# Performance work log

Hardware: AMD Instinct MI355X
Metric: run time of the kernel (lower is better)

Reference implementation:

```python
import jax, jax.numpy as jnp
import numpy as np

BETA = 0.25


def setup_inputs() -> dict:
    key = jax.random.key(0)
    k1, k2, k3 = jax.random.split(key, 3)
    B, T, D, K = 4, 2048, 512, 16384
    z_e = jax.random.normal(k1, (B, T, D), dtype=jnp.float32)
    codebook = jax.random.normal(k2, (K, D), dtype=jnp.float32)  # frozen embedding
    # nn.Linear(D, D, bias=False) weight, scaled like kaiming-uniform magnitude
    W = jax.random.normal(k3, (D, D), dtype=jnp.float32) * (1.0 / np.sqrt(D))
    return {"z_e": z_e, "codebook": codebook, "W": W}


def reference(z_e, codebook, W):
    B, T, D = z_e.shape
    # effective codebook: Linear(codebook) = codebook @ W.T   -> (K, D)
    eff = jnp.matmul(codebook, W.T)
    z_flat = z_e.reshape(-1, D)  # (N, D)
    # squared euclidean distances (argmin-equivalent to cdist p=2)
    d2 = (
        jnp.sum(z_flat * z_flat, axis=1, keepdims=True)  # (N,1)
        - 2.0 * jnp.matmul(z_flat, eff.T)                  # (N,K)
        + jnp.sum(eff * eff, axis=1)[None, :]              # (1,K)
    )
    code_indices = jnp.argmin(d2, axis=1)  # (N,)
    z_q = eff[code_indices].reshape(B, T, D)
    loss_w = jnp.mean((jax.lax.stop_gradient(z_e) - z_q) ** 2)
    loss_commit = BETA * jnp.mean((z_e - jax.lax.stop_gradient(z_q)) ** 2)
    total_loss = loss_w + loss_commit
    # straight-through estimator
    z_q_out = z_e + jax.lax.stop_gradient(z_q - z_e)
    return z_q_out, total_loss, code_indices.reshape(B, T)
```

## Files before the change

kernel.cpp:

```cpp
#include <hip/hip_runtime.h>
#include <stdint.h>


#define N_ROWS 8192
#define DIM    512
#define K_CB   16384
#define TILE_F16 16384
#define HALF_F16 8192
#define KT_EFF 24
#define KT_D   8
#define PAN_D   ((size_t)KT_D * TILE_F16)
#define RMARGIN 4.0f

typedef _Float16 f16x8 __attribute__((ext_vector_type(8)));
typedef float f32x4 __attribute__((ext_vector_type(4)));

#define FENCE() asm volatile("" ::: "memory")
#define BARRIER() do { FENCE(); __builtin_amdgcn_s_barrier(); FENCE(); } while (0)
#define VMCNT(n) asm volatile("s_waitcnt vmcnt(" #n ")" ::: "memory")

__device__ __forceinline__ void gload_lds16(const void* g, void* l) {
  __builtin_amdgcn_global_load_lds(
      (const __attribute__((address_space(1))) uint32_t*)g,
      (__attribute__((address_space(3))) uint32_t*)l, 16, 0, 0);
}


__device__ __forceinline__ void stage_half(const _Float16* src, _Float16* ldsb,
                                           int w, int lane) {
  const _Float16* s = src + w * 512 + lane * 8;
  _Float16* l = ldsb + w * 512;
  gload_lds16(s, l);
  gload_lds16(s + 4096, l + 4096);
}

template <int MQ>
__device__ __forceinline__ void read_a(const _Float16* At, int wr, int lh, int lq,
                                       f16x8 af[4][2]) {
#pragma unroll
  for (int m2 = 0; m2 < 4; ++m2) {
    const int row = wr * 128 + (MQ * 4 + m2) * 16 + lh;
    const int half = row >> 7, r = row & 127;
#pragma unroll
    for (int kk = 0; kk < 2; ++kk) {
      const int kblk = kk * 4 + lq;
      af[m2][kk] = *reinterpret_cast<const f16x8*>(
          &At[(((size_t)(half * 8 + kblk)) * 128 + r) * 8]);
    }
  }
}

template <int NQ>
__device__ __forceinline__ void read_b(const _Float16* Bt, int wc, int lh, int lq,
                                       f16x8 bf[4][2]) {
#pragma unroll
  for (int n2 = 0; n2 < 2; ++n2) {
    const int row = wc * 64 + (NQ * 2 + n2) * 16 + lh;
    const int half = row >> 7, r = row & 127;
#pragma unroll
    for (int kk = 0; kk < 2; ++kk) {
      const int kblk = kk * 4 + lq;
      bf[NQ * 2 + n2][kk] = *reinterpret_cast<const f16x8*>(
          &Bt[(((size_t)(half * 8 + kblk)) * 128 + r) * 8]);
    }
  }
}

template <int MQ, int NQ>
__device__ __forceinline__ void mfma_phase(const f16x8 af[4][2],
                                           const f16x8 bf[4][2],
                                           f32x4 acc[8][4]) {
  __builtin_amdgcn_s_setprio(1);
#pragma unroll
  for (int m2 = 0; m2 < 4; ++m2)
#pragma unroll
    for (int n2 = 0; n2 < 2; ++n2)
#pragma unroll
      for (int kk = 0; kk < 2; ++kk)
        acc[MQ * 4 + m2][NQ * 2 + n2] = __builtin_amdgcn_mfma_f32_16x16x32_f16(
            af[m2][kk], bf[NQ * 2 + n2][kk], acc[MQ * 4 + m2][NQ * 2 + n2], 0, 0, 0);
  __builtin_amdgcn_s_setprio(0);
}

__device__ __forceinline__ void pipeline8(
    const _Float16* Abase, const _Float16* Bbase,
    _Float16 (&lds)[4][TILE_F16], f32x4 (&acc)[8][4],
    int w, int lane, int wr, int wc, int lh, int lq, int NT) {
  f16x8 af[4][2], bf[4][2];
  stage_half(Abase, &lds[0][0], w, lane);
  stage_half(Abase + HALF_F16, &lds[0][HALF_F16], w, lane);
  stage_half(Bbase, &lds[1][0], w, lane);
  stage_half(Bbase + HALF_F16, &lds[1][HALF_F16], w, lane);
  stage_half(Bbase + TILE_F16, &lds[3][0], w, lane);
  stage_half(Bbase + TILE_F16 + HALF_F16, &lds[3][HALF_F16], w, lane);
  stage_half(Abase + TILE_F16, &lds[2][0], w, lane);
  VMCNT(6);
  BARRIER();
  for (int t = 0; t < NT; ++t) {
    const int s = t & 1;
    const _Float16* At = &lds[s * 2 + 0][0];
    const _Float16* Bt = &lds[s * 2 + 1][0];
    read_a<0>(At, wr, lh, lq, af);
    read_b<0>(Bt, wc, lh, lq, bf);
    if (t + 1 < NT)
      stage_half(Abase + (size_t)(t + 1) * TILE_F16 + HALF_F16,
                 &lds[(s ^ 1) * 2][HALF_F16], w, lane);
    BARRIER();
    mfma_phase<0, 0>(af, bf, acc);
    BARRIER();
    read_b<1>(Bt, wc, lh, lq, bf);
    BARRIER();
    mfma_phase<0, 1>(af, bf, acc);
    BARRIER();
    read_a<1>(At, wr, lh, lq, af);
    if (t + 2 < NT)
      stage_half(Bbase + (size_t)(t + 2) * TILE_F16, &lds[s * 2 + 1][0], w, lane);
    BARRIER();
    mfma_phase<1, 1>(af, bf, acc);
    BARRIER();
    if (t + 2 < NT) {
      stage_half(Bbase + (size_t)(t + 2) * TILE_F16 + HALF_F16,
                 &lds[s * 2 + 1][HALF_F16], w, lane);
      stage_half(Abase + (size_t)(t + 2) * TILE_F16, &lds[s * 2][0], w, lane);
    }
    BARRIER();
    mfma_phase<1, 0>(af, bf, acc);
    if (t == NT - 2) { VMCNT(0); } else { VMCNT(6); }
    BARRIER();
  }
}

__global__ __launch_bounds__(256) void split_tiled_kernel(
    const float* __restrict__ S, _Float16* __restrict__ T, int resid_limb) {
  const int b = blockIdx.x;
  const int mp = b / 48;
  const int r1 = b % 48;
  const int kt = r1 >> 1, half = r1 & 1;
  const int limb = kt >> 3;
  const int ksrc = (kt & 7) * 64;
  const bool resid = (limb == resid_limb);
  const int t = threadIdx.x;
  _Float16* dst = T + ((size_t)(mp * KT_EFF + kt) * 2 + half) * HALF_F16;
#pragma unroll
  for (int cc = 0; cc < 4; ++cc) {
    const int ci = cc * 256 + t;
    const int kblk = ci >> 7, row = ci & 127;
    const int m = mp * 256 + half * 128 + row;
    const float* src = &S[(size_t)m * DIM + ksrc + kblk * 8];
    float4 x0 = *reinterpret_cast<const float4*>(src);
    float4 x1 = *reinterpret_cast<const float4*>(src + 4);
    const float xs[8] = {x0.x, x0.y, x0.z, x0.w, x1.x, x1.y, x1.z, x1.w};
    f16x8 o;
    if (!resid) {
#pragma unroll
      for (int j = 0; j < 8; ++j) o[j] = (_Float16)xs[j];
    } else {
#pragma unroll
      for (int j = 0; j < 8; ++j) {
        _Float16 h = (_Float16)xs[j];
        o[j] = (_Float16)(xs[j] - (float)h);
      }
    }
    *reinterpret_cast<f16x8*>(&dst[(size_t)ci * 8]) = o;
  }
}

__global__ __launch_bounds__(256) void split1_kernel(
    const float* __restrict__ S, _Float16* __restrict__ T) {
  const int b = blockIdx.x;
  const int p = b >> 4;
  const int r1 = b & 15;
  const int kt = r1 >> 1, half = r1 & 1;
  const int ksrc = kt * 64;
  const int t = threadIdx.x;
  _Float16* dst = T + ((size_t)(p * KT_D + kt) * 2 + half) * HALF_F16;
#pragma unroll
  for (int cc = 0; cc < 4; ++cc) {
    const int ci = cc * 256 + t;
    const int kblk = ci >> 7, row = ci & 127;
    const int m = p * 256 + half * 128 + row;
    const float* src = &S[(size_t)m * DIM + ksrc + kblk * 8];
    float4 x0 = *reinterpret_cast<const float4*>(src);
    float4 x1 = *reinterpret_cast<const float4*>(src + 4);
    const float xs[8] = {x0.x, x0.y, x0.z, x0.w, x1.x, x1.y, x1.z, x1.w};
    f16x8 o;
#pragma unroll
    for (int j = 0; j < 8; ++j) o[j] = (_Float16)xs[j];
    *reinterpret_cast<f16x8*>(&dst[(size_t)ci * 8]) = o;
  }
}

__global__ __launch_bounds__(256) void effgemm128_kernel(
    const _Float16* __restrict__ CpT, const _Float16* __restrict__ WpT,
    float* __restrict__ eff, _Float16* __restrict__ BpT) {
  __shared__ __align__(16) _Float16 lbuf[2][2][HALF_F16];
  const int tid = threadIdx.x;
  const int w = tid >> 6, lane = tid & 63;
  const int lh = lane & 15, lq = lane >> 4;
  const int wr = w >> 1, wc = w & 1;
  const int bid = blockIdx.x;
  const int nb = bid & 3, mh = bid >> 2;
  const int pA = mh >> 1, hA = mh & 1;
  const int pB = nb >> 1, hB = nb & 1;
  f32x4 acc[4][4] = {};

  auto stage = [&](int kt, int buf) {
    const _Float16* a = CpT + (((size_t)pA * KT_EFF + kt) * 2 + hA) * HALF_F16;
    const _Float16* b = WpT + (((size_t)pB * KT_EFF + kt) * 2 + hB) * HALF_F16;
#pragma unroll
    for (int i = 0; i < 4; ++i) {
      const int off = i * 2048 + w * 512;
      gload_lds16(a + off + lane * 8, &lbuf[buf][0][off]);
      gload_lds16(b + off + lane * 8, &lbuf[buf][1][off]);
    }
  };

  stage(0, 0);
  for (int kt = 0; kt < KT_EFF; ++kt) {
    __syncthreads();
    if (kt + 1 < KT_EFF) stage(kt + 1, (kt + 1) & 1);
    const _Float16* At = &lbuf[kt & 1][0][0];
    const _Float16* Bt = &lbuf[kt & 1][1][0];
    f16x8 af[4][2], bf[4][2];
#pragma unroll
    for (int mf = 0; mf < 4; ++mf) {
      const int r = wr * 64 + mf * 16 + lh;
#pragma unroll
      for (int kk = 0; kk < 2; ++kk)
        af[mf][kk] = *reinterpret_cast<const f16x8*>(
            &At[((kk * 4 + lq) * 128 + r) * 8]);
    }
#pragma unroll
    for (int nf = 0; nf < 4; ++nf) {
      const int r = wc * 64 + nf * 16 + lh;
#pragma unroll
      for (int kk = 0; kk < 2; ++kk)
        bf[nf][kk] = *reinterpret_cast<const f16x8*>(
            &Bt[((kk * 4 + lq) * 128 + r) * 8]);
    }
    __builtin_amdgcn_s_setprio(1);
#pragma unroll
    for (int mf = 0; mf < 4; ++mf)
#pragma unroll
      for (int nf = 0; nf < 4; ++nf)
#pragma unroll
        for (int kk = 0; kk < 2; ++kk)
          acc[mf][nf] = __builtin_amdgcn_mfma_f32_16x16x32_f16(
              af[mf][kk], bf[nf][kk], acc[mf][nf], 0, 0, 0);
    __builtin_amdgcn_s_setprio(0);
  }

#pragma unroll
  for (int mf = 0; mf < 4; ++mf)
#pragma unroll
    for (int nf = 0; nf < 4; ++nf)
#pragma unroll
      for (int j = 0; j < 4; ++j) {
        const int rl = wr * 64 + mf * 16 + lq * 4 + j;
        const int cl = wc * 64 + nf * 16 + lh;
        const int row = mh * 128 + rl;
        const int col = nb * 128 + cl;
        const float v = acc[mf][nf][j];
        eff[(size_t)row * DIM + col] = v;
        const int ktd = col >> 6, kblk = (col >> 3) & 7, ce = col & 7;
        BpT[((((size_t)(row >> 8) * KT_D + ktd) * 2 + ((row >> 7) & 1)) * 8 + kblk)
                * 1024 + (row & 127) * 8 + ce] = (_Float16)v;
      }
}

__global__ __launch_bounds__(256) void effnorm_kernel(
    const float* __restrict__ E, float* __restrict__ En) {
  const int w = threadIdx.x >> 6;
  const int lane = threadIdx.x & 63;
  const int row = blockIdx.x * 4 + w;
  const float* er = &E[(size_t)row * DIM];
  float s = 0.f;
#pragma unroll
  for (int k = 0; k < DIM / 64; ++k) {
    float v = er[lane + k * 64];
    s = fmaf(v, v, s);
  }
#pragma unroll
  for (int o = 32; o; o >>= 1) s += __shfl_down(s, o, 64);
  if (lane == 0) En[row] = s;
}

__global__ __launch_bounds__(512) void dist1_kernel(
    const _Float16* __restrict__ ApT, const _Float16* __restrict__ BpT,
    const float* __restrict__ En, float* __restrict__ gv,
    unsigned* __restrict__ gmask) {
  __shared__ __align__(16) _Float16 lds[4][TILE_F16];
  const int tid = threadIdx.x;
  const int w = tid >> 6, lane = tid & 63;
  const int lh = lane & 15, lq = lane >> 4;
  const int wr = w >> 2, wc = w & 3;
  const int bid = blockIdx.x;
  const int xcd = bid & 7, c = bid >> 3;
  const int np = xcd * 8 + (c & 7);
  const int mp = c >> 3;
  f32x4 acc[8][4] = {};
  pipeline8(ApT + (size_t)mp * PAN_D, BpT + (size_t)np * PAN_D, lds, acc,
            w, lane, wr, wc, lh, lq, KT_D);
  float en[4];
#pragma unroll
  for (int nf = 0; nf < 4; ++nf)
    en[nf] = En[np * 256 + wc * 64 + nf * 16 + lh];
#pragma unroll
  for (int mf = 0; mf < 8; ++mf) {
#pragma unroll
    for (int j = 0; j < 4; ++j) {
      const float s0 = fmaf(-2.f, acc[mf][0][j], en[0]);
      const float s1 = fmaf(-2.f, acc[mf][1][j], en[1]);
      const float s2 = fmaf(-2.f, acc[mf][2][j], en[2]);
      const float s3 = fmaf(-2.f, acc[mf][3][j], en[3]);
      float v0 = fminf(s0, s1);
      float v1 = fminf(s2, s3);
#pragma unroll
      for (int m = 1; m < 16; m <<= 1) {
        v0 = fminf(v0, __shfl_xor(v0, m, 64));
        v1 = fminf(v1, __shfl_xor(v1, m, 64));
      }
      const unsigned long long b0 = __ballot(s0 <= v0 + RMARGIN);
      const unsigned long long b1 = __ballot(s1 <= v0 + RMARGIN);
      const unsigned long long b2 = __ballot(s2 <= v1 + RMARGIN);
      const unsigned long long b3 = __ballot(s3 <= v1 + RMARGIN);
      if (lh == 0) {
        const int row = mp * 256 + wr * 128 + mf * 16 + lq * 4 + j;
        float* gp = &gv[(size_t)row * 512 + np * 8 + wc * 2];
        gp[0] = v0; gp[1] = v1;
        const unsigned w0 = (unsigned)((b0 >> (lq * 16)) & 0xFFFFull) |
                            ((unsigned)((b1 >> (lq * 16)) & 0xFFFFull) << 16);
        const unsigned w1 = (unsigned)((b2 >> (lq * 16)) & 0xFFFFull) |
                            ((unsigned)((b3 >> (lq * 16)) & 0xFFFFull) << 16);
        unsigned* mq = &gmask[(size_t)row * 512 + np * 8 + wc * 2];
        mq[0] = w0; mq[1] = w1;
      }
    }
  }
}

__global__ __launch_bounds__(256) void flag_kernel(
    const float* __restrict__ gv, int* __restrict__ fcnt,
    unsigned short* __restrict__ flist) {
  const int t = threadIdx.x;
  const int w = t >> 6, lane = t & 63;
  const int row = blockIdx.x * 4 + w;
  float v[8];
#pragma unroll
  for (int i = 0; i < 8; ++i) v[i] = gv[(size_t)row * 512 + i * 64 + lane];
  float A = v[0];
#pragma unroll
  for (int i = 1; i < 8; ++i) A = fminf(A, v[i]);
#pragma unroll
  for (int m = 1; m < 64; m <<= 1) A = fminf(A, __shfl_xor(A, m, 64));
  __shared__ int cnt[4];
  __shared__ unsigned short lst[4][64];
  if (lane == 0) cnt[w] = 0;
  __syncthreads();
  const float thr = A + RMARGIN;
#pragma unroll
  for (int i = 0; i < 8; ++i) {
    if (v[i] <= thr) {
      int p = atomicAdd(&cnt[w], 1);
      if (p < 64) lst[w][p] = (unsigned short)(i * 64 + lane);
    }
  }
  __syncthreads();
  const int cn = cnt[w];
  if (lane == 0) fcnt[row] = (cn > 64) ? -1 : cn;
  if (lane < cn && lane < 64) flist[(size_t)row * 64 + lane] = lst[w][lane];
}

__global__ __launch_bounds__(256) void refine_kernel(
    const float* __restrict__ Z, const float* __restrict__ E,
    const float* __restrict__ En, const int* __restrict__ fcnt,
    const unsigned short* __restrict__ flist, const unsigned* __restrict__ gmask,
    float* __restrict__ zq, float* __restrict__ out_idx,
    float* __restrict__ ploss) {
  const int row = blockIdx.x;
  const int t = threadIdx.x;
  const int w = t >> 6, lane = t & 63;
  const int hl = lane & 31;
  const int hi = lane >> 5;
  __shared__ float zrow[512];
  __shared__ unsigned short glist[512];
  __shared__ float bvs[4];
  __shared__ int bis[4];
  __shared__ int sidx;
  __shared__ float wsum[4];
  if (t < 128)
    ((float4*)zrow)[t] = ((const float4*)(Z + (size_t)row * 512))[t];
  const int cr = fcnt[row];
  int ng;
  if (cr < 0) {
    glist[t] = (unsigned short)t;
    glist[t + 256] = (unsigned short)(t + 256);
    ng = 512;
  } else {
    ng = cr;
    if (t < cr) glist[t] = flist[(size_t)row * 64 + t];
  }
  float4 zr0, zr1, zr2, zr3;
  {
    const float4* zp = (const float4*)(Z + (size_t)row * 512 + hl * 16);
    zr0 = zp[0]; zr1 = zp[1]; zr2 = zp[2]; zr3 = zp[3];
  }
  __syncthreads();

  float bv = 3.0e38f;
  int bi = 2147483647;
  for (int q = w; q < ng; q += 4) {
    const int g = glist[q];
    unsigned m = gmask[(size_t)row * 512 + g];
    while (m) {
      const int c0 = __builtin_ctz(m);
      m &= m - 1;
      int c1 = -1;
      if (m) { c1 = __builtin_ctz(m); m &= m - 1; }
      const int cl = hi ? c1 : c0;
      const bool act = (cl >= 0);
      const int col = g * 32 + (act ? cl : c0);
      const float4* er = (const float4*)(E + (size_t)col * 512 + hl * 16);
      const float4 e0 = er[0], e1 = er[1], e2 = er[2], e3 = er[3];
      float p = 0.f;
      p = fmaf(zr0.x, e0.x, p); p = fmaf(zr0.y, e0.y, p);
      p = fmaf(zr0.z, e0.z, p); p = fmaf(zr0.w, e0.w, p);
      p = fmaf(zr1.x, e1.x, p); p = fmaf(zr1.y, e1.y, p);
      p = fmaf(zr1.z, e1.z, p); p = fmaf(zr1.w, e1.w, p);
      p = fmaf(zr2.x, e2.x, p); p = fmaf(zr2.y, e2.y, p);
      p = fmaf(zr2.z, e2.z, p); p = fmaf(zr2.w, e2.w, p);
      p = fmaf(zr3.x, e3.x, p); p = fmaf(zr3.y, e3.y, p);
      p = fmaf(zr3.z, e3.z, p); p = fmaf(zr3.w, e3.w, p);
#pragma unroll
      for (int s2 = 1; s2 < 32; s2 <<= 1) p += __shfl_xor(p, s2, 64);
      const float v = fmaf(-2.f, p, En[col]);
      if (act && (v < bv || (v == bv && col < bi))) { bv = v; bi = col; }
    }
  }
#pragma unroll
  for (int s2 = 1; s2 < 64; s2 <<= 1) {
    const float v2 = __shfl_xor(bv, s2, 64);
    const int i2 = __shfl_xor(bi, s2, 64);
    if (v2 < bv || (v2 == bv && i2 < bi)) { bv = v2; bi = i2; }
  }
  if (lane == 0) { bvs[w] = bv; bis[w] = bi; }
  __syncthreads();
  if (t == 0) {
    float fb = bvs[0];
    int fi = bis[0];
#pragma unroll
    for (int i = 1; i < 4; ++i)
      if (bvs[i] < fb || (bvs[i] == fb && bis[i] < fi)) { fb = bvs[i]; fi = bis[i]; }
    sidx = fi;
  }
  __syncthreads();
  const int idx = sidx;

  float s = 0.f;
  const float* erow = E + (size_t)idx * 512;
#pragma unroll
  for (int d0 = 0; d0 < 512; d0 += 256) {
    const int d = d0 + t;
    const float e = erow[d];
    const float z = zrow[d];
    zq[(size_t)row * 512 + d] = e;
    const float df = z - e;
    s = fmaf(df, df, s);
  }
#pragma unroll
  for (int o = 32; o; o >>= 1) s += __shfl_down(s, o, 64);
  if ((t & 63) == 0) wsum[t >> 6] = s;
  __syncthreads();
  if (t == 0) {
    ploss[row] = wsum[0] + wsum[1] + wsum[2] + wsum[3];
    out_idx[row] = (float)idx;
  }
}

__global__ __launch_bounds__(256) void loss_final_kernel(
    const float* __restrict__ ploss, float* __restrict__ out_loss) {
  const int t = threadIdx.x;
  double s = 0.0;
  for (int i = t; i < N_ROWS; i += 256) s += (double)ploss[i];
#pragma unroll
  for (int o = 32; o; o >>= 1) s += __shfl_down(s, o, 64);
  __shared__ double ds[4];
  if ((t & 63) == 0) ds[t >> 6] = s;
  __syncthreads();
  if (t == 0) {
    double tot = ds[0] + ds[1] + ds[2] + ds[3];
    out_loss[0] = (float)(1.25 * tot / ((double)N_ROWS * (double)DIM));
  }
}


extern "C" void kernel_launch(void* const* d_in, const int* in_sizes, int n_in,
                              void* d_out, int out_size, void* d_ws, size_t ws_size,
                              hipStream_t stream) {
  const float* z_e      = (const float*)d_in[0];
  const float* codebook = (const float*)d_in[1];
  const float* W        = (const float*)d_in[2];
  float* out = (float*)d_out;
  char* ws = (char*)d_ws;

  float*          eff     = (float*)(ws);
  float*          effnorm = (float*)(ws + 33554432);
  _Float16*       WpT     = (_Float16*)(ws + 33619968);
  int*            fcnt    = (int*)(ws + 35192832);
  unsigned short* flist   = (unsigned short*)(ws + 35225600);
  float*          ploss   = (float*)(ws + 36274176);
  _Float16*       CpT     = (_Float16*)(ws + 36306944);
  float*          gv      = (float*)(ws + 36306944);
  _Float16*       ApT     = (_Float16*)(ws + 53084160);
  unsigned*       gmask   = (unsigned*)(ws + 61472768);
  _Float16*       BpT     = (_Float16*)(ws + 86638592);

  float* out_zq   = out;
  float* out_loss = out + (size_t)N_ROWS * DIM;
  float* out_idx  = out + (size_t)N_ROWS * DIM + 1;

  split_tiled_kernel<<<64 * 48, 256, 0, stream>>>(codebook, CpT, 2);
  split_tiled_kernel<<<2 * 48, 256, 0, stream>>>(W, WpT, 1);
  effgemm128_kernel<<<512, 256, 0, stream>>>(CpT, WpT, eff, BpT);
  effnorm_kernel<<<K_CB / 4, 256, 0, stream>>>(eff, effnorm);
  split1_kernel<<<32 * 16, 256, 0, stream>>>(z_e, ApT);
  dist1_kernel<<<2048, 512, 0, stream>>>(ApT, BpT, effnorm, gv, gmask);
  flag_kernel<<<N_ROWS / 4, 256, 0, stream>>>(gv, fcnt, flist);
  refine_kernel<<<N_ROWS, 256, 0, stream>>>(z_e, eff, effnorm, fcnt, flist,
                                            gmask, out_zq, out_idx, ploss);
  loss_final_kernel<<<1, 256, 0, stream>>>(ploss, out_loss);
}
```

Baseline: 293.0 us.

## Switch distance GEMM to 32x32x16 MFMA with single-phase K-step pipeline

Rewrites the dist1 kernel's main loop to use 32x32x16 f16 MFMA tiles instead of 16x16x32. All A and B fragments for a K-tile are loaded in one go, replacing the four read/compute phases that each needed two barriers. The aim is fewer LDS reads and barriers per tile and higher MFMA throughput per instruction. The epilogue now reduces over 32 lanes per row, which takes more shuffles per value, and the larger fragment arrays raise register pressure.

```diff
diff --git a/kernel.cpp b/kernel.cpp
--- a/kernel.cpp
+++ b/kernel.cpp
@@ -14,6 +14,7 @@
 
 typedef _Float16 f16x8 __attribute__((ext_vector_type(8)));
 typedef float f32x4 __attribute__((ext_vector_type(4)));
+typedef float f32x16 __attribute__((ext_vector_type(16)));
 
 #define FENCE() asm volatile("" ::: "memory")
 #define BARRIER() do { FENCE(); __builtin_amdgcn_s_barrier(); FENCE(); } while (0)
@@ -32,102 +33,6 @@
   _Float16* l = ldsb + w * 512;
   gload_lds16(s, l);
   gload_lds16(s + 4096, l + 4096);
-}
-
-template <int MQ>
-__device__ __forceinline__ void read_a(const _Float16* At, int wr, int lh, int lq,
-                                       f16x8 af[4][2]) {
-#pragma unroll
-  for (int m2 = 0; m2 < 4; ++m2) {
-    const int row = wr * 128 + (MQ * 4 + m2) * 16 + lh;
-    const int half = row >> 7, r = row & 127;
-#pragma unroll
-    for (int kk = 0; kk < 2; ++kk) {
-      const int kblk = kk * 4 + lq;
-      af[m2][kk] = *reinterpret_cast<const f16x8*>(
-          &At[(((size_t)(half * 8 + kblk)) * 128 + r) * 8]);
-    }
-  }
-}
-
-template <int NQ>
-__device__ __forceinline__ void read_b(const _Float16* Bt, int wc, int lh, int lq,
-                                       f16x8 bf[4][2]) {
-#pragma unroll
-  for (int n2 = 0; n2 < 2; ++n2) {
-    const int row = wc * 64 + (NQ * 2 + n2) * 16 + lh;
-    const int half = row >> 7, r = row & 127;
-#pragma unroll
-    for (int kk = 0; kk < 2; ++kk) {
-      const int kblk = kk * 4 + lq;
-      bf[NQ * 2 + n2][kk] = *reinterpret_cast<const f16x8*>(
-          &Bt[(((size_t)(half * 8 + kblk)) * 128 + r) * 8]);
-    }
-  }
-}
-
-template <int MQ, int NQ>
-__device__ __forceinline__ void mfma_phase(const f16x8 af[4][2],
-                                           const f16x8 bf[4][2],
-                                           f32x4 acc[8][4]) {
-  __builtin_amdgcn_s_setprio(1);
-#pragma unroll
-  for (int m2 = 0; m2 < 4; ++m2)
-#pragma unroll
-    for (int n2 = 0; n2 < 2; ++n2)
-#pragma unroll
-      for (int kk = 0; kk < 2; ++kk)
-        acc[MQ * 4 + m2][NQ * 2 + n2] = __builtin_amdgcn_mfma_f32_16x16x32_f16(
-            af[m2][kk], bf[NQ * 2 + n2][kk], acc[MQ * 4 + m2][NQ * 2 + n2], 0, 0, 0);
-  __builtin_amdgcn_s_setprio(0);
-}
-
-__device__ __forceinline__ void pipeline8(
-    const _Float16* Abase, const _Float16* Bbase,
-    _Float16 (&lds)[4][TILE_F16], f32x4 (&acc)[8][4],
-    int w, int lane, int wr, int wc, int lh, int lq, int NT) {
-  f16x8 af[4][2], bf[4][2];
-  stage_half(Abase, &lds[0][0], w, lane);
-  stage_half(Abase + HALF_F16, &lds[0][HALF_F16], w, lane);
-  stage_half(Bbase, &lds[1][0], w, lane);
-  stage_half(Bbase + HALF_F16, &lds[1][HALF_F16], w, lane);
-  stage_half(Bbase + TILE_F16, &lds[3][0], w, lane);
-  stage_half(Bbase + TILE_F16 + HALF_F16, &lds[3][HALF_F16], w, lane);
-  stage_half(Abase + TILE_F16, &lds[2][0], w, lane);
-  VMCNT(6);
-  BARRIER();
-  for (int t = 0; t < NT; ++t) {
-    const int s = t & 1;
-    const _Float16* At = &lds[s * 2 + 0][0];
-    const _Float16* Bt = &lds[s * 2 + 1][0];
-    read_a<0>(At, wr, lh, lq, af);
-    read_b<0>(Bt, wc, lh, lq, bf);
-    if (t + 1 < NT)
-      stage_half(Abase + (size_t)(t + 1) * TILE_F16 + HALF_F16,
-                 &lds[(s ^ 1) * 2][HALF_F16], w, lane);
-    BARRIER();
-    mfma_phase<0, 0>(af, bf, acc);
-    BARRIER();
-    read_b<1>(Bt, wc, lh, lq, bf);
-    BARRIER();
-    mfma_phase<0, 1>(af, bf, acc);
-    BARRIER();
-    read_a<1>(At, wr, lh, lq, af);
-    if (t + 2 < NT)
-      stage_half(Bbase + (size_t)(t + 2) * TILE_F16, &lds[s * 2 + 1][0], w, lane);
-    BARRIER();
-    mfma_phase<1, 1>(af, bf, acc);
-    BARRIER();
-    if (t + 2 < NT) {
-      stage_half(Bbase + (size_t)(t + 2) * TILE_F16 + HALF_F16,
-                 &lds[s * 2 + 1][HALF_F16], w, lane);
-      stage_half(Abase + (size_t)(t + 2) * TILE_F16, &lds[s * 2][0], w, lane);
-    }
-    BARRIER();
-    mfma_phase<1, 0>(af, bf, acc);
-    if (t == NT - 2) { VMCNT(0); } else { VMCNT(6); }
-    BARRIER();
-  }
 }
 
 __global__ __launch_bounds__(256) void split_tiled_kernel(
@@ -292,51 +197,95 @@
   __shared__ __align__(16) _Float16 lds[4][TILE_F16];
   const int tid = threadIdx.x;
   const int w = tid >> 6, lane = tid & 63;
-  const int lh = lane & 15, lq = lane >> 4;
+  const int l31 = lane & 31, kh = lane >> 5;
   const int wr = w >> 2, wc = w & 3;
   const int bid = blockIdx.x;
   const int xcd = bid & 7, c = bid >> 3;
   const int np = xcd * 8 + (c & 7);
   const int mp = c >> 3;
-  f32x4 acc[8][4] = {};
-  pipeline8(ApT + (size_t)mp * PAN_D, BpT + (size_t)np * PAN_D, lds, acc,
-            w, lane, wr, wc, lh, lq, KT_D);
-  float en[4];
-#pragma unroll
-  for (int nf = 0; nf < 4; ++nf)
-    en[nf] = En[np * 256 + wc * 64 + nf * 16 + lh];
-#pragma unroll
-  for (int mf = 0; mf < 8; ++mf) {
-#pragma unroll
-    for (int j = 0; j < 4; ++j) {
-      const float s0 = fmaf(-2.f, acc[mf][0][j], en[0]);
-      const float s1 = fmaf(-2.f, acc[mf][1][j], en[1]);
-      const float s2 = fmaf(-2.f, acc[mf][2][j], en[2]);
-      const float s3 = fmaf(-2.f, acc[mf][3][j], en[3]);
-      float v0 = fminf(s0, s1);
-      float v1 = fminf(s2, s3);
-#pragma unroll
-      for (int m = 1; m < 16; m <<= 1) {
-        v0 = fminf(v0, __shfl_xor(v0, m, 64));
-        v1 = fminf(v1, __shfl_xor(v1, m, 64));
+  const _Float16* Ab = ApT + (size_t)mp * PAN_D;
+  const _Float16* Bb = BpT + (size_t)np * PAN_D;
+
+  float en[2];
+  en[0] = En[np * 256 + wc * 64 + l31];
+  en[1] = En[np * 256 + wc * 64 + 32 + l31];
+
+  f32x16 acc[4][2] = {};
+  f16x8 a32[4][4], b32[2][4];
+
+  stage_half(Ab, &lds[0][0], w, lane);
+  stage_half(Ab + HALF_F16, &lds[0][HALF_F16], w, lane);
+  stage_half(Bb, &lds[1][0], w, lane);
+  stage_half(Bb + HALF_F16, &lds[1][HALF_F16], w, lane);
+  stage_half(Bb + TILE_F16, &lds[3][0], w, lane);
+  stage_half(Bb + TILE_F16 + HALF_F16, &lds[3][HALF_F16], w, lane);
+  stage_half(Ab + TILE_F16, &lds[2][0], w, lane);
+  VMCNT(6);
+  BARRIER();
+
+  for (int t = 0; t < KT_D; ++t) {
+    const int s = t & 1;
+    const _Float16* At = &lds[s * 2 + 0][0];
+    const _Float16* Bt = &lds[s * 2 + 1][0];
+    if (t + 1 < KT_D)
+      stage_half(Ab + (size_t)(t + 1) * TILE_F16 + HALF_F16,
+                 &lds[(s ^ 1) * 2][HALF_F16], w, lane);
+#pragma unroll
+    for (int mi = 0; mi < 4; ++mi)
+#pragma unroll
+      for (int k16 = 0; k16 < 4; ++k16)
+        a32[mi][k16] = *reinterpret_cast<const f16x8*>(
+            &At[(((wr * 8 + k16 * 2 + kh) * 128) + mi * 32 + l31) * 8]);
+    {
+      const int halfb = wc >> 1, rb = (wc & 1) * 64 + l31;
+#pragma unroll
+      for (int ni = 0; ni < 2; ++ni)
+#pragma unroll
+        for (int k16 = 0; k16 < 4; ++k16)
+          b32[ni][k16] = *reinterpret_cast<const f16x8*>(
+              &Bt[(((halfb * 8 + k16 * 2 + kh) * 128) + rb + ni * 32) * 8]);
+    }
+    BARRIER();
+    __builtin_amdgcn_s_setprio(1);
+#pragma unroll
+    for (int k16 = 0; k16 < 4; ++k16)
+#pragma unroll
+      for (int mi = 0; mi < 4; ++mi)
+#pragma unroll
+        for (int ni = 0; ni < 2; ++ni)
+          acc[mi][ni] = __builtin_amdgcn_mfma_f32_32x32x16_f16(
+              a32[mi][k16], b32[ni][k16], acc[mi][ni], 0, 0, 0);
+    __builtin_amdgcn_s_setprio(0);
+    if (t + 2 < KT_D) {
+      stage_half(Bb + (size_t)(t + 2) * TILE_F16, &lds[s * 2 + 1][0], w, lane);
+      stage_half(Bb + (size_t)(t + 2) * TILE_F16 + HALF_F16,
+                 &lds[s * 2 + 1][HALF_F16], w, lane);
+      stage_half(Ab + (size_t)(t + 2) * TILE_F16, &lds[s * 2][0], w, lane);
+    }
+    if (t == KT_D - 2) { VMCNT(0); BARRIER(); }
+    else if (t + 1 < KT_D) { VMCNT(6); BARRIER(); }
+  }
+
+#pragma unroll
+  for (int mi = 0; mi < 4; ++mi)
+#pragma unroll
+    for (int ni = 0; ni < 2; ++ni) {
+#pragma unroll
+      for (int reg = 0; reg < 16; ++reg) {
+        const float sc = fmaf(-2.f, acc[mi][ni][reg], en[ni]);
+        float g = sc;
+#pragma unroll
+        for (int m = 1; m < 32; m <<= 1) g = fminf(g, __shfl_xor(g, m, 64));
+        const unsigned long long b = __ballot(sc <= g + RMARGIN);
+        if (l31 == 0) {
+          const int row = mp * 256 + wr * 128 + mi * 32 +
+                          (reg & 3) + 8 * (reg >> 2) + 4 * kh;
+          const int gidx = np * 8 + wc * 2 + ni;
+          gv[(size_t)row * 512 + gidx] = g;
+          gmask[(size_t)row * 512 + gidx] = (unsigned)(b >> (kh * 32));
+        }
       }
-      const unsigned long long b0 = __ballot(s0 <= v0 + RMARGIN);
-      const unsigned long long b1 = __ballot(s1 <= v0 + RMARGIN);
-      const unsigned long long b2 = __ballot(s2 <= v1 + RMARGIN);
-      const unsigned long long b3 = __ballot(s3 <= v1 + RMARGIN);
-      if (lh == 0) {
-        const int row = mp * 256 + wr * 128 + mf * 16 + lq * 4 + j;
-        float* gp = &gv[(size_t)row * 512 + np * 8 + wc * 2];
-        gp[0] = v0; gp[1] = v1;
-        const unsigned w0 = (unsigned)((b0 >> (lq * 16)) & 0xFFFFull) |
-                            ((unsigned)((b1 >> (lq * 16)) & 0xFFFFull) << 16);
-        const unsigned w1 = (unsigned)((b2 >> (lq * 16)) & 0xFFFFull) |
-                            ((unsigned)((b3 >> (lq * 16)) & 0xFFFFull) << 16);
-        unsigned* mq = &gmask[(size_t)row * 512 + np * 8 + wc * 2];
-        mq[0] = w0; mq[1] = w1;
-      }
-    }
-  }
+    }
 }
 
 __global__ __launch_bounds__(256) void flag_kernel(
```

After: 531.3 us. 1.81x slower.

## Fuse flag pass into refine kernel with one wavefront per row

Applied to the files above, without the earlier changes.

Removes the separate flag kernel. The refine kernel now handles one row per wavefront, reads the per-group minima itself, and uses ballots to walk the candidate groups directly instead of building a list in shared memory. This drops a kernel launch, the fcnt/flist round trip through global memory, and the block-level syncs, at the cost of each row being scanned by 64 lanes rather than 256 threads. It also vectorises the gv/gmask stores as float2/uint2 and reorders the MFMA loops so kk is outermost.

```diff
diff --git a/kernel.cpp b/kernel.cpp
--- a/kernel.cpp
+++ b/kernel.cpp
@@ -72,11 +72,11 @@
                                            f32x4 acc[8][4]) {
   __builtin_amdgcn_s_setprio(1);
 #pragma unroll
-  for (int m2 = 0; m2 < 4; ++m2)
-#pragma unroll
-    for (int n2 = 0; n2 < 2; ++n2)
-#pragma unroll
-      for (int kk = 0; kk < 2; ++kk)
+  for (int kk = 0; kk < 2; ++kk)
+#pragma unroll
+    for (int m2 = 0; m2 < 4; ++m2)
+#pragma unroll
+      for (int n2 = 0; n2 < 2; ++n2)
         acc[MQ * 4 + m2][NQ * 2 + n2] = __builtin_amdgcn_mfma_f32_16x16x32_f16(
             af[m2][kk], bf[NQ * 2 + n2][kk], acc[MQ * 4 + m2][NQ * 2 + n2], 0, 0, 0);
   __builtin_amdgcn_s_setprio(0);
@@ -240,11 +240,11 @@
     }
     __builtin_amdgcn_s_setprio(1);
 #pragma unroll
-    for (int mf = 0; mf < 4; ++mf)
-#pragma unroll
-      for (int nf = 0; nf < 4; ++nf)
-#pragma unroll
-        for (int kk = 0; kk < 2; ++kk)
+    for (int kk = 0; kk < 2; ++kk)
+#pragma unroll
+      for (int mf = 0; mf < 4; ++mf)
+#pragma unroll
+        for (int nf = 0; nf < 4; ++nf)
           acc[mf][nf] = __builtin_amdgcn_mfma_f32_16x16x32_f16(
               af[mf][kk], bf[nf][kk], acc[mf][nf], 0, 0, 0);
     __builtin_amdgcn_s_setprio(0);
@@ -326,115 +326,78 @@
       const unsigned long long b3 = __ballot(s3 <= v1 + RMARGIN);
       if (lh == 0) {
         const int row = mp * 256 + wr * 128 + mf * 16 + lq * 4 + j;
-        float* gp = &gv[(size_t)row * 512 + np * 8 + wc * 2];
-        gp[0] = v0; gp[1] = v1;
         const unsigned w0 = (unsigned)((b0 >> (lq * 16)) & 0xFFFFull) |
                             ((unsigned)((b1 >> (lq * 16)) & 0xFFFFull) << 16);
         const unsigned w1 = (unsigned)((b2 >> (lq * 16)) & 0xFFFFull) |
                             ((unsigned)((b3 >> (lq * 16)) & 0xFFFFull) << 16);
-        unsigned* mq = &gmask[(size_t)row * 512 + np * 8 + wc * 2];
-        mq[0] = w0; mq[1] = w1;
+        float2* gp = (float2*)&gv[(size_t)row * 512 + np * 8 + wc * 2];
+        *gp = make_float2(v0, v1);
+        uint2* mq = (uint2*)&gmask[(size_t)row * 512 + np * 8 + wc * 2];
+        *mq = make_uint2(w0, w1);
       }
     }
   }
-}
-
-__global__ __launch_bounds__(256) void flag_kernel(
-    const float* __restrict__ gv, int* __restrict__ fcnt,
-    unsigned short* __restrict__ flist) {
-  const int t = threadIdx.x;
-  const int w = t >> 6, lane = t & 63;
-  const int row = blockIdx.x * 4 + w;
-  float v[8];
-#pragma unroll
-  for (int i = 0; i < 8; ++i) v[i] = gv[(size_t)row * 512 + i * 64 + lane];
-  float A = v[0];
-#pragma unroll
-  for (int i = 1; i < 8; ++i) A = fminf(A, v[i]);
-#pragma unroll
-  for (int m = 1; m < 64; m <<= 1) A = fminf(A, __shfl_xor(A, m, 64));
-  __shared__ int cnt[4];
-  __shared__ unsigned short lst[4][64];
-  if (lane == 0) cnt[w] = 0;
-  __syncthreads();
-  const float thr = A + RMARGIN;
-#pragma unroll
-  for (int i = 0; i < 8; ++i) {
-    if (v[i] <= thr) {
-      int p = atomicAdd(&cnt[w], 1);
-      if (p < 64) lst[w][p] = (unsigned short)(i * 64 + lane);
-    }
-  }
-  __syncthreads();
-  const int cn = cnt[w];
-  if (lane == 0) fcnt[row] = (cn > 64) ? -1 : cn;
-  if (lane < cn && lane < 64) flist[(size_t)row * 64 + lane] = lst[w][lane];
 }
 
 __global__ __launch_bounds__(256) void refine_kernel(
     const float* __restrict__ Z, const float* __restrict__ E,
-    const float* __restrict__ En, const int* __restrict__ fcnt,
-    const unsigned short* __restrict__ flist, const unsigned* __restrict__ gmask,
-    float* __restrict__ zq, float* __restrict__ out_idx,
-    float* __restrict__ ploss) {
-  const int row = blockIdx.x;
-  const int t = threadIdx.x;
-  const int w = t >> 6, lane = t & 63;
+    const float* __restrict__ En, const float* __restrict__ gv,
+    const unsigned* __restrict__ gmask, float* __restrict__ zq,
+    float* __restrict__ out_idx, float* __restrict__ ploss) {
+  const int row = blockIdx.x * 4 + (threadIdx.x >> 6);
+  const int lane = threadIdx.x & 63;
   const int hl = lane & 31;
   const int hi = lane >> 5;
-  __shared__ float zrow[512];
-  __shared__ unsigned short glist[512];
-  __shared__ float bvs[4];
-  __shared__ int bis[4];
-  __shared__ int sidx;
-  __shared__ float wsum[4];
-  if (t < 128)
-    ((float4*)zrow)[t] = ((const float4*)(Z + (size_t)row * 512))[t];
-  const int cr = fcnt[row];
-  int ng;
-  if (cr < 0) {
-    glist[t] = (unsigned short)t;
-    glist[t + 256] = (unsigned short)(t + 256);
-    ng = 512;
-  } else {
-    ng = cr;
-    if (t < cr) glist[t] = flist[(size_t)row * 64 + t];
-  }
+
+  float v[8];
+#pragma unroll
+  for (int i = 0; i < 8; ++i) v[i] = gv[(size_t)row * 512 + i * 64 + lane];
+  float A = fminf(fminf(fminf(v[0], v[1]), fminf(v[2], v[3])),
+                  fminf(fminf(v[4], v[5]), fminf(v[6], v[7])));
+#pragma unroll
+  for (int m = 1; m < 64; m <<= 1) A = fminf(A, __shfl_xor(A, m, 64));
+  const float thr = A + RMARGIN;
+
   float4 zr0, zr1, zr2, zr3;
   {
     const float4* zp = (const float4*)(Z + (size_t)row * 512 + hl * 16);
     zr0 = zp[0]; zr1 = zp[1]; zr2 = zp[2]; zr3 = zp[3];
   }
-  __syncthreads();
 
   float bv = 3.0e38f;
   int bi = 2147483647;
-  for (int q = w; q < ng; q += 4) {
-    const int g = glist[q];
-    unsigned m = gmask[(size_t)row * 512 + g];
-    while (m) {
-      const int c0 = __builtin_ctz(m);
-      m &= m - 1;
-      int c1 = -1;
-      if (m) { c1 = __builtin_ctz(m); m &= m - 1; }
-      const int cl = hi ? c1 : c0;
-      const bool act = (cl >= 0);
-      const int col = g * 32 + (act ? cl : c0);
-      const float4* er = (const float4*)(E + (size_t)col * 512 + hl * 16);
-      const float4 e0 = er[0], e1 = er[1], e2 = er[2], e3 = er[3];
-      float p = 0.f;
-      p = fmaf(zr0.x, e0.x, p); p = fmaf(zr0.y, e0.y, p);
-      p = fmaf(zr0.z, e0.z, p); p = fmaf(zr0.w, e0.w, p);
-      p = fmaf(zr1.x, e1.x, p); p = fmaf(zr1.y, e1.y, p);
-      p = fmaf(zr1.z, e1.z, p); p = fmaf(zr1.w, e1.w, p);
-      p = fmaf(zr2.x, e2.x, p); p = fmaf(zr2.y, e2.y, p);
-      p = fmaf(zr2.z, e2.z, p); p = fmaf(zr2.w, e2.w, p);
-      p = fmaf(zr3.x, e3.x, p); p = fmaf(zr3.y, e3.y, p);
-      p = fmaf(zr3.z, e3.z, p); p = fmaf(zr3.w, e3.w, p);
-#pragma unroll
-      for (int s2 = 1; s2 < 32; s2 <<= 1) p += __shfl_xor(p, s2, 64);
-      const float v = fmaf(-2.f, p, En[col]);
-      if (act && (v < bv || (v == bv && col < bi))) { bv = v; bi = col; }
+#pragma unroll 1
+  for (int i = 0; i < 8; ++i) {
+    unsigned long long bm = __ballot(v[i] <= thr);
+    while (bm) {
+      const int l = __builtin_ctzll(bm);
+      bm &= bm - 1;
+      const int g = i * 64 + l;
+      unsigned m = gmask[(size_t)row * 512 + g];
+      while (m) {
+        const int c0 = __builtin_ctz(m);
+        m &= m - 1;
+        int c1 = -1;
+        if (m) { c1 = __builtin_ctz(m); m &= m - 1; }
+        const int cl = hi ? c1 : c0;
+        const bool act = (cl >= 0);
+        const int col = g * 32 + (act ? cl : c0);
+        const float4* er = (const float4*)(E + (size_t)col * 512 + hl * 16);
+        const float4 e0 = er[0], e1 = er[1], e2 = er[2], e3 = er[3];
+        float p = 0.f;
+        p = fmaf(zr0.x, e0.x, p); p = fmaf(zr0.y, e0.y, p);
+        p = fmaf(zr0.z, e0.z, p); p = fmaf(zr0.w, e0.w, p);
+        p = fmaf(zr1.x, e1.x, p); p = fmaf(zr1.y, e1.y, p);
+        p = fmaf(zr1.z, e1.z, p); p = fmaf(zr1.w, e1.w, p);
+        p = fmaf(zr2.x, e2.x, p); p = fmaf(zr2.y, e2.y, p);
+        p = fmaf(zr2.z, e2.z, p); p = fmaf(zr2.w, e2.w, p);
+        p = fmaf(zr3.x, e3.x, p); p = fmaf(zr3.y, e3.y, p);
+        p = fmaf(zr3.z, e3.z, p); p = fmaf(zr3.w, e3.w, p);
+#pragma unroll
+        for (int s2 = 1; s2 < 32; s2 <<= 1) p += __shfl_xor(p, s2, 64);
+        const float vv = fmaf(-2.f, p, En[col]);
+        if (act && (vv < bv || (vv == bv && col < bi))) { bv = vv; bi = col; }
+      }
     }
   }
 #pragma unroll
@@ -443,36 +406,23 @@
     const int i2 = __shfl_xor(bi, s2, 64);
     if (v2 < bv || (v2 == bv && i2 < bi)) { bv = v2; bi = i2; }
   }
-  if (lane == 0) { bvs[w] = bv; bis[w] = bi; }
-  __syncthreads();
-  if (t == 0) {
-    float fb = bvs[0];
-    int fi = bis[0];
-#pragma unroll
-    for (int i = 1; i < 4; ++i)
-      if (bvs[i] < fb || (bvs[i] == fb && bis[i] < fi)) { fb = bvs[i]; fi = bis[i]; }
-    sidx = fi;
-  }
-  __syncthreads();
-  const int idx = sidx;
-
+  const int idx = bi;
+
+  const float4* e4 = (const float4*)(E + (size_t)idx * 512 + lane * 8);
+  const float4* z4 = (const float4*)(Z + (size_t)row * 512 + lane * 8);
+  float4* q4 = (float4*)(zq + (size_t)row * 512 + lane * 8);
+  const float4 ea = e4[0], eb = e4[1];
+  const float4 za = z4[0], zb = z4[1];
+  q4[0] = ea; q4[1] = eb;
   float s = 0.f;
-  const float* erow = E + (size_t)idx * 512;
-#pragma unroll
-  for (int d0 = 0; d0 < 512; d0 += 256) {
-    const int d = d0 + t;
-    const float e = erow[d];
-    const float z = zrow[d];
-    zq[(size_t)row * 512 + d] = e;
-    const float df = z - e;
-    s = fmaf(df, df, s);
-  }
+  s = fmaf(za.x - ea.x, za.x - ea.x, s); s = fmaf(za.y - ea.y, za.y - ea.y, s);
+  s = fmaf(za.z - ea.z, za.z - ea.z, s); s = fmaf(za.w - ea.w, za.w - ea.w, s);
+  s = fmaf(zb.x - eb.x, zb.x - eb.x, s); s = fmaf(zb.y - eb.y, zb.y - eb.y, s);
+  s = fmaf(zb.z - eb.z, zb.z - eb.z, s); s = fmaf(zb.w - eb.w, zb.w - eb.w, s);
 #pragma unroll
   for (int o = 32; o; o >>= 1) s += __shfl_down(s, o, 64);
-  if ((t & 63) == 0) wsum[t >> 6] = s;
-  __syncthreads();
-  if (t == 0) {
-    ploss[row] = wsum[0] + wsum[1] + wsum[2] + wsum[3];
+  if (lane == 0) {
+    ploss[row] = s;
     out_idx[row] = (float)idx;
   }
 }
@@ -506,8 +456,6 @@
   float*          eff     = (float*)(ws);
   float*          effnorm = (float*)(ws + 33554432);
   _Float16*       WpT     = (_Float16*)(ws + 33619968);
-  int*            fcnt    = (int*)(ws + 35192832);
-  unsigned short* flist   = (unsigned short*)(ws + 35225600);
   float*          ploss   = (float*)(ws + 36274176);
   _Float16*       CpT     = (_Float16*)(ws + 36306944);
   float*          gv      = (float*)(ws + 36306944);
@@ -525,8 +473,7 @@
   effnorm_kernel<<<K_CB / 4, 256, 0, stream>>>(eff, effnorm);
   split1_kernel<<<32 * 16, 256, 0, stream>>>(z_e, ApT);
   dist1_kernel<<<2048, 512, 0, stream>>>(ApT, BpT, effnorm, gv, gmask);
-  flag_kernel<<<N_ROWS / 4, 256, 0, stream>>>(gv, fcnt, flist);
-  refine_kernel<<<N_ROWS, 256, 0, stream>>>(z_e, eff, effnorm, fcnt, flist,
-                                            gmask, out_zq, out_idx, ploss);
+  refine_kernel<<<N_ROWS / 4, 256, 0, stream>>>(z_e, eff, effnorm, gv, gmask,
+                                                out_zq, out_idx, ploss);
   loss_final_kernel<<<1, 256, 0, stream>>>(ploss, out_loss);
 }
```

Measured after the change: 282.0 us, median of 2. 3.8% less time.
